# Optimization experiments

Hardware: AMD Instinct MI355X
Metric: run time of the kernel (lower is better)

Reference implementation:

```python
import jax, jax.numpy as jnp
import numpy as np

T, B, E, H = 2048, 4, 1024, 16
D = E // H  # head_dim = 64


def setup_inputs() -> dict:
    key = jax.random.key(0)
    k1, k2, k3, k4 = jax.random.split(key, 4)
    x = jax.random.normal(k1, (T, B, E), dtype=jnp.float32)
    # xavier-ish init scale
    Wqkv = jax.random.normal(k2, (3 * E, E), dtype=jnp.float32) * (1.0 / np.sqrt(2.0 * E))
    Wo = jax.random.normal(k3, (E, E), dtype=jnp.float32) * (1.0 / np.sqrt(E))
    key_padding_mask = jax.random.randint(k4, (B, T), 0, 2).astype(jnp.bool_)  # True = pad
    return {"x": x, "Wqkv": Wqkv, "Wo": Wo, "key_padding_mask": key_padding_mask}


def reference(x, Wqkv, Wo, key_padding_mask):
    t, b, e = x.shape
    h, d = H, E // H
    # fused QKV projection (bias=False)
    qkv = jnp.einsum('tbe,fe->tbf', x, Wqkv).reshape(t, b, 3, h, d)
    # chunk along the 3-axis, then permute to (B, H, T, D)
    q = jnp.transpose(qkv[:, :, 0], (1, 2, 0, 3))
    k = jnp.transpose(qkv[:, :, 1], (1, 2, 0, 3))
    v = jnp.transpose(qkv[:, :, 2], (1, 2, 0, 3))
    # SDPA with default scale 1/sqrt(head_dim); additive -inf mask on padded keys
    scale = 1.0 / jnp.sqrt(jnp.asarray(d, dtype=x.dtype))
    scores = jnp.einsum('bhtd,bhsd->bhts', q, k) * scale
    scores = jnp.where(key_padding_mask[:, None, None, :], -jnp.inf, scores)
    probs = jax.nn.softmax(scores, axis=-1)
    ctx = jnp.einsum('bhts,bhsd->bhtd', probs, v)  # (B,H,T,D)
    ctx = jnp.transpose(ctx, (0, 2, 1, 3)).reshape(b, t, e)  # (B,T,E)
    out = jnp.einsum('bte,fe->btf', ctx, Wo)  # out_proj, bias=False
    return jnp.transpose(out, (1, 0, 2))  # back to (T,B,E)
```

## Files before the change

kernel.cpp:

```cpp
#include <hip/hip_runtime.h>

typedef unsigned short u16;
typedef __bf16 bf16x8 __attribute__((ext_vector_type(8)));
typedef unsigned short u16x8 __attribute__((ext_vector_type(8)));
typedef unsigned short u16x4 __attribute__((ext_vector_type(4)));
typedef float f32x4 __attribute__((ext_vector_type(4)));

__device__ __forceinline__ f32x4 mfma16(u16x8 a, u16x8 b, f32x4 c) {
    return __builtin_amdgcn_mfma_f32_16x16x32_bf16(
        __builtin_bit_cast(bf16x8, a), __builtin_bit_cast(bf16x8, b), c, 0, 0, 0);
}

__device__ __forceinline__ u16 f2b(float f) {
    unsigned int u = __builtin_bit_cast(unsigned int, f);
    return (u16)((u + 0x7fffu + ((u >> 16) & 1u)) >> 16);
}

__device__ __forceinline__ f32x4 zero4() { f32x4 z = {0.f, 0.f, 0.f, 0.f}; return z; }

typedef __attribute__((address_space(1))) const unsigned int gas_u32;
typedef __attribute__((address_space(3))) unsigned int las_u32;
__device__ __forceinline__ void gload16(const u16* g, u16* l) {
    __builtin_amdgcn_global_load_lds((gas_u32*)g, (las_u32*)l, 16, 0, 0);
}

__global__ __launch_bounds__(256) void cvt_bf16_kernel(const float* __restrict__ in,
                                                       u16* __restrict__ out, int n) {
    int i = (blockIdx.x * 256 + threadIdx.x) * 4;
    if (i >= n) return;
    float4 v = *reinterpret_cast<const float4*>(in + i);
    u16x4 o;
    o.x = f2b(v.x); o.y = f2b(v.y); o.z = f2b(v.z); o.w = f2b(v.w);
    *reinterpret_cast<u16x4*>(out + i) = o;
}

__global__ void detect_mask_kernel(const unsigned char* __restrict__ m, int* __restrict__ flag) {
    __shared__ int any;
    if (threadIdx.x == 0) any = 0;
    __syncthreads();
    int acc = 0;
    for (int i = threadIdx.x; i < 8192; i += 256)
        if (i & 3) acc |= m[i];
    if (acc) atomicOr(&any, 1);
    __syncthreads();
    if (threadIdx.x == 0) *flag = any ? 0 : 1;
}

template <int EPI>
__global__ __launch_bounds__(256)
void gemm_bt_kernel(const u16* __restrict__ A, const u16* __restrict__ Bt,
                    int M, int N, int K,
                    u16* __restrict__ qo, u16* __restrict__ ko, u16* __restrict__ vo,
                    float* __restrict__ fo) {
    constexpr int BK = 32;
    __shared__ u16 Al[128 * BK];
    __shared__ u16 Bl[128 * BK];
    int tid = threadIdx.x;
    int wave = tid >> 6, lane = tid & 63;
    int l15 = lane & 15, l16 = lane >> 4;
    int wr = wave >> 1, wc = wave & 1;
    int bx = blockIdx.x, by = blockIdx.y;

    int c0 = tid, c1 = tid + 256;
    const u16* gA0 = A + (size_t)(by * 128 + (c0 >> 2)) * K + (c0 & 3) * 8;
    const u16* gA1 = A + (size_t)(by * 128 + (c1 >> 2)) * K + (c1 & 3) * 8;
    const u16* gB0 = Bt + (size_t)(bx * 128 + (c0 >> 2)) * K + (c0 & 3) * 8;
    const u16* gB1 = Bt + (size_t)(bx * 128 + (c1 >> 2)) * K + (c1 & 3) * 8;
    u16* lA0 = Al + c0 * 8; u16* lA1 = Al + c1 * 8;
    u16* lB0 = Bl + c0 * 8; u16* lB1 = Bl + c1 * 8;

    f32x4 acc[4][4];
#pragma unroll
    for (int m = 0; m < 4; m++)
#pragma unroll
        for (int n = 0; n < 4; n++) acc[m][n] = zero4();

    for (int k0 = 0; k0 < K; k0 += BK) {
        __syncthreads();
        gload16(gA0 + k0, lA0);
        gload16(gA1 + k0, lA1);
        gload16(gB0 + k0, lB0);
        gload16(gB1 + k0, lB1);
        __syncthreads();
        u16x8 af[4], bfr[4];
#pragma unroll
        for (int m = 0; m < 4; m++)
            af[m] = *(const u16x8*)&Al[(wr * 64 + m * 16 + l15) * BK + l16 * 8];
#pragma unroll
        for (int n = 0; n < 4; n++)
            bfr[n] = *(const u16x8*)&Bl[(wc * 64 + n * 16 + l15) * BK + l16 * 8];
#pragma unroll
        for (int m = 0; m < 4; m++)
#pragma unroll
            for (int n = 0; n < 4; n++) acc[m][n] = mfma16(af[m], bfr[n], acc[m][n]);
    }

#pragma unroll
    for (int m = 0; m < 4; m++) {
#pragma unroll
        for (int j = 0; j < 4; j++) {
            int row = by * 128 + wr * 64 + m * 16 + l16 * 4 + j;
#pragma unroll
            for (int n = 0; n < 4; n++) {
                int col = bx * 128 + wc * 64 + n * 16 + l15;
                float val = acc[m][n][j];
                if constexpr (EPI == 0) {
                    int chunk = col >> 10, h = (col >> 6) & 15, d = col & 63;
                    int t = row >> 2, bI = row & 3;
                    if (chunk == 0) val *= 0.18033688011112042f;
                    u16* dst = (chunk == 0) ? qo : (chunk == 1) ? ko : vo;
                    dst[((size_t)(bI * 16 + h) * 2048 + t) * 64 + d] = f2b(val);
                } else {
                    fo[(size_t)row * N + col] = val;
                }
            }
        }
    }
}

__global__ __launch_bounds__(256)
void attn_kernel(const u16* __restrict__ Qg, const u16* __restrict__ Kg,
                 const u16* __restrict__ Vg, const void* __restrict__ maskp,
                 const int* __restrict__ flag, u16* __restrict__ ctx) {
    __shared__ u16 Kl[32 * 72];
    __shared__ u16 Vt[64 * 40];
    __shared__ u16 Pl[4][32 * 40];

    int tid = threadIdx.x;
    int wave = tid >> 6, lane = tid & 63;
    int l15 = lane & 15, l16 = lane >> 4;
    int bh = blockIdx.y;
    int b = bh >> 4, h = bh & 15;
    size_t base = (size_t)bh * 2048 * 64;
    int q0 = blockIdx.x * 128 + wave * 32;

    int isInt = *flag;
    const unsigned char* m8 = (const unsigned char*)maskp;
    const int* m32 = (const int*)maskp;

    u16x8 aq[2][2];
#pragma unroll
    for (int qb = 0; qb < 2; qb++)
#pragma unroll
        for (int ks = 0; ks < 2; ks++)
            aq[qb][ks] = *(const u16x8*)(Qg + base + (size_t)(q0 + qb * 16 + l15) * 64 +
                                         ks * 32 + l16 * 8);

    f32x4 acc_o[2][4];
    float mrun[2][4], plsum[2][4];
#pragma unroll
    for (int qb = 0; qb < 2; qb++) {
#pragma unroll
        for (int db = 0; db < 4; db++) acc_o[qb][db] = zero4();
#pragma unroll
        for (int j = 0; j < 4; j++) { mrun[qb][j] = -1e30f; plsum[qb][j] = 0.f; }
    }

    int srow = tid >> 3, schunk = tid & 7;

    for (int s0 = 0; s0 < 2048; s0 += 32) {
        u16x8 kv = *(const u16x8*)(Kg + base + (size_t)(s0 + srow) * 64 + schunk * 8);
        u16x8 vv = *(const u16x8*)(Vg + base + (size_t)(s0 + srow) * 64 + schunk * 8);
        __syncthreads();
        *(u16x8*)&Kl[srow * 72 + schunk * 8] = kv;
#pragma unroll
        for (int s = 0; s < 8; s++) {
            int i = (srow + schunk + s) & 7;
            Vt[(schunk * 8 + i) * 40 + srow] = vv[i];
        }
        __syncthreads();

        int ki = b * 2048 + s0 + l15;
        int pad0 = isInt ? (m32[ki] != 0) : (m8[ki] != 0);
        int pad1 = isInt ? (m32[ki + 16] != 0) : (m8[ki + 16] != 0);

        f32x4 sa[2][2];
        sa[0][0] = zero4(); sa[0][1] = zero4(); sa[1][0] = zero4(); sa[1][1] = zero4();
#pragma unroll
        for (int kb = 0; kb < 2; kb++)
#pragma unroll
            for (int ks = 0; ks < 2; ks++) {
                u16x8 bk = *(const u16x8*)&Kl[(kb * 16 + l15) * 72 + ks * 32 + l16 * 8];
                sa[0][kb] = mfma16(aq[0][ks], bk, sa[0][kb]);
                sa[1][kb] = mfma16(aq[1][ks], bk, sa[1][kb]);
            }

#pragma unroll
        for (int qb = 0; qb < 2; qb++) {
            float s0v[4], s1v[4];
            float gl = -1e30f;
#pragma unroll
            for (int j = 0; j < 4; j++) {
                s0v[j] = pad0 ? -1e30f : sa[qb][0][j];
                s1v[j] = pad1 ? -1e30f : sa[qb][1][j];
                gl = fmaxf(gl, fmaxf(s0v[j], s1v[j]) - mrun[qb][j]);
            }
            if (__any(gl > 4.0f)) {
                float tm[4];
#pragma unroll
                for (int j = 0; j < 4; j++) tm[j] = fmaxf(s0v[j], s1v[j]);
#pragma unroll
                for (int j = 0; j < 4; j++) {
                    tm[j] = fmaxf(tm[j], __shfl_xor(tm[j], 1));
                    tm[j] = fmaxf(tm[j], __shfl_xor(tm[j], 2));
                    tm[j] = fmaxf(tm[j], __shfl_xor(tm[j], 4));
                    tm[j] = fmaxf(tm[j], __shfl_xor(tm[j], 8));
                }
#pragma unroll
                for (int j = 0; j < 4; j++) {
                    float mnew = fmaxf(mrun[qb][j], tm[j]);
                    float sc = exp2f(mrun[qb][j] - mnew);
                    mrun[qb][j] = mnew;
                    plsum[qb][j] *= sc;
#pragma unroll
                    for (int db = 0; db < 4; db++) acc_o[qb][db][j] *= sc;
                }
            }
#pragma unroll
            for (int j = 0; j < 4; j++) {
                float p0 = exp2f(s0v[j] - mrun[qb][j]);
                float p1 = exp2f(s1v[j] - mrun[qb][j]);
                int prow = qb * 16 + l16 * 4 + j;
                Pl[wave][prow * 40 + l15] = f2b(p0);
                Pl[wave][prow * 40 + 16 + l15] = f2b(p1);
                plsum[qb][j] += p0 + p1;
            }
        }

#pragma unroll
        for (int qb = 0; qb < 2; qb++) {
            u16x8 ap = *(const u16x8*)&Pl[wave][(qb * 16 + l15) * 40 + l16 * 8];
#pragma unroll
            for (int db = 0; db < 4; db++) {
                u16x8 bv = *(const u16x8*)&Vt[(db * 16 + l15) * 40 + l16 * 8];
                acc_o[qb][db] = mfma16(ap, bv, acc_o[qb][db]);
            }
        }
    }

#pragma unroll
    for (int qb = 0; qb < 2; qb++)
#pragma unroll
        for (int j = 0; j < 4; j++) {
            float rs = plsum[qb][j];
            rs += __shfl_xor(rs, 1);
            rs += __shfl_xor(rs, 2);
            rs += __shfl_xor(rs, 4);
            rs += __shfl_xor(rs, 8);
            float inv = 1.0f / rs;
            int qg = q0 + qb * 16 + l16 * 4 + j;
            size_t mrow = (size_t)qg * 4 + b;
#pragma unroll
            for (int db = 0; db < 4; db++)
                ctx[mrow * 1024 + h * 64 + db * 16 + l15] = f2b(acc_o[qb][db][j] * inv);
        }
}

extern "C" void kernel_launch(void* const* d_in, const int* in_sizes, int n_in,
                              void* d_out, int out_size, void* d_ws, size_t ws_size,
                              hipStream_t stream) {
    const float* x = (const float*)d_in[0];
    const float* wqkv = (const float*)d_in[1];
    const float* wo = (const float*)d_in[2];
    const void* mask = d_in[3];
    float* out = (float*)d_out;

    char* ws = (char*)d_ws;
    int* flag = (int*)ws;
    u16* xb = (u16*)(ws + 16);
    u16* wqkvb = xb + 8388608;
    u16* wob = wqkvb + 3145728;
    u16* qw = wob + 1048576;
    u16* kw = qw + 8388608;
    u16* vw = kw + 8388608;
    u16* ctx = xb;

    cvt_bf16_kernel<<<8192, 256, 0, stream>>>(x, xb, 8388608);
    cvt_bf16_kernel<<<3072, 256, 0, stream>>>(wqkv, wqkvb, 3145728);
    cvt_bf16_kernel<<<1024, 256, 0, stream>>>(wo, wob, 1048576);
    detect_mask_kernel<<<1, 256, 0, stream>>>((const unsigned char*)mask, flag);

    gemm_bt_kernel<0><<<dim3(24, 64), 256, 0, stream>>>(xb, wqkvb, 8192, 3072, 1024,
                                                        qw, kw, vw, nullptr);
    attn_kernel<<<dim3(16, 64), 256, 0, stream>>>(qw, kw, vw, mask, flag, ctx);
    gemm_bt_kernel<1><<<dim3(8, 64), 256, 0, stream>>>(ctx, wob, 8192, 1024, 1024,
                                                       nullptr, nullptr, nullptr, out);
}
```

Measured before the change: 473.8 us.

## Use LDS transpose reads for V, prefetch K/V, widen GEMM BK to 64

The GEMM K-tile grows from 32 to 64, so there are half as many sync and load rounds and each tile feeds two MFMA sub-steps. In attention, V is no longer scattered element by element into a transposed LDS buffer. It is stored as row chunks and read with ds_read_b64_tr_b16 transpose loads. The next K/V tile is loaded from global memory into registers during the current iteration to hide latency. The online-softmax rescale threshold is loosened from 4 to 8, which skips more rescales but lets the exponentials grow larger before rescaling. The explicit lgkmcnt waits and sched barriers may serialize the transpose loads.

```diff
diff --git a/kernel.cpp b/kernel.cpp
--- a/kernel.cpp
+++ b/kernel.cpp
@@ -22,6 +22,12 @@
 typedef __attribute__((address_space(3))) unsigned int las_u32;
 __device__ __forceinline__ void gload16(const u16* g, u16* l) {
     __builtin_amdgcn_global_load_lds((gas_u32*)g, (las_u32*)l, 16, 0, 0);
+}
+
+__device__ __forceinline__ u16x4 tr16(unsigned off) {
+    u16x4 r;
+    asm volatile("ds_read_b64_tr_b16 %0, %1" : "=v"(r) : "v"(off));
+    return r;
 }
 
 __global__ __launch_bounds__(256) void cvt_bf16_kernel(const float* __restrict__ in,
@@ -52,22 +58,24 @@
                     int M, int N, int K,
                     u16* __restrict__ qo, u16* __restrict__ ko, u16* __restrict__ vo,
                     float* __restrict__ fo) {
-    constexpr int BK = 32;
-    __shared__ u16 Al[128 * BK];
-    __shared__ u16 Bl[128 * BK];
+    constexpr int BK = 64;
+    __shared__ __align__(16) u16 Al[128 * BK];
+    __shared__ __align__(16) u16 Bl[128 * BK];
     int tid = threadIdx.x;
     int wave = tid >> 6, lane = tid & 63;
     int l15 = lane & 15, l16 = lane >> 4;
     int wr = wave >> 1, wc = wave & 1;
     int bx = blockIdx.x, by = blockIdx.y;
 
-    int c0 = tid, c1 = tid + 256;
-    const u16* gA0 = A + (size_t)(by * 128 + (c0 >> 2)) * K + (c0 & 3) * 8;
-    const u16* gA1 = A + (size_t)(by * 128 + (c1 >> 2)) * K + (c1 & 3) * 8;
-    const u16* gB0 = Bt + (size_t)(bx * 128 + (c0 >> 2)) * K + (c0 & 3) * 8;
-    const u16* gB1 = Bt + (size_t)(bx * 128 + (c1 >> 2)) * K + (c1 & 3) * 8;
-    u16* lA0 = Al + c0 * 8; u16* lA1 = Al + c1 * 8;
-    u16* lB0 = Bl + c0 * 8; u16* lB1 = Bl + c1 * 8;
+    const u16* gA[4]; const u16* gB[4]; u16* lA[4]; u16* lB[4];
+#pragma unroll
+    for (int q = 0; q < 4; q++) {
+        int c = tid + q * 256;
+        gA[q] = A + (size_t)(by * 128 + (c >> 3)) * K + (c & 7) * 8;
+        gB[q] = Bt + (size_t)(bx * 128 + (c >> 3)) * K + (c & 7) * 8;
+        lA[q] = Al + c * 8;
+        lB[q] = Bl + c * 8;
+    }
 
     f32x4 acc[4][4];
 #pragma unroll
@@ -77,22 +85,26 @@
 
     for (int k0 = 0; k0 < K; k0 += BK) {
         __syncthreads();
-        gload16(gA0 + k0, lA0);
-        gload16(gA1 + k0, lA1);
-        gload16(gB0 + k0, lB0);
-        gload16(gB1 + k0, lB1);
+#pragma unroll
+        for (int q = 0; q < 4; q++) {
+            gload16(gA[q] + k0, lA[q]);
+            gload16(gB[q] + k0, lB[q]);
+        }
         __syncthreads();
-        u16x8 af[4], bfr[4];
-#pragma unroll
-        for (int m = 0; m < 4; m++)
-            af[m] = *(const u16x8*)&Al[(wr * 64 + m * 16 + l15) * BK + l16 * 8];
-#pragma unroll
-        for (int n = 0; n < 4; n++)
-            bfr[n] = *(const u16x8*)&Bl[(wc * 64 + n * 16 + l15) * BK + l16 * 8];
-#pragma unroll
-        for (int m = 0; m < 4; m++)
-#pragma unroll
-            for (int n = 0; n < 4; n++) acc[m][n] = mfma16(af[m], bfr[n], acc[m][n]);
+#pragma unroll
+        for (int ks = 0; ks < 2; ks++) {
+            u16x8 af[4], bfr[4];
+#pragma unroll
+            for (int m = 0; m < 4; m++)
+                af[m] = *(const u16x8*)&Al[(wr * 64 + m * 16 + l15) * BK + ks * 32 + l16 * 8];
+#pragma unroll
+            for (int n = 0; n < 4; n++)
+                bfr[n] = *(const u16x8*)&Bl[(wc * 64 + n * 16 + l15) * BK + ks * 32 + l16 * 8];
+#pragma unroll
+            for (int m = 0; m < 4; m++)
+#pragma unroll
+                for (int n = 0; n < 4; n++) acc[m][n] = mfma16(af[m], bfr[n], acc[m][n]);
+        }
     }
 
 #pragma unroll
@@ -122,9 +134,9 @@
 void attn_kernel(const u16* __restrict__ Qg, const u16* __restrict__ Kg,
                  const u16* __restrict__ Vg, const void* __restrict__ maskp,
                  const int* __restrict__ flag, u16* __restrict__ ctx) {
-    __shared__ u16 Kl[32 * 72];
-    __shared__ u16 Vt[64 * 40];
-    __shared__ u16 Pl[4][32 * 40];
+    __shared__ __align__(16) u16 Kl[32 * 72];
+    __shared__ __align__(128) u16 Vs[2048];
+    __shared__ __align__(16) u16 Pl[4][32 * 40];
 
     int tid = threadIdx.x;
     int wave = tid >> 6, lane = tid & 63;
@@ -157,17 +169,23 @@
     }
 
     int srow = tid >> 3, schunk = tid & 7;
-
-    for (int s0 = 0; s0 < 2048; s0 += 32) {
-        u16x8 kv = *(const u16x8*)(Kg + base + (size_t)(s0 + srow) * 64 + schunk * 8);
-        u16x8 vv = *(const u16x8*)(Vg + base + (size_t)(s0 + srow) * 64 + schunk * 8);
+    const u16* kg = Kg + base + (size_t)srow * 64 + schunk * 8;
+    const u16* vg = Vg + base + (size_t)srow * 64 + schunk * 8;
+    u16* kldst = &Kl[srow * 72 + schunk * 8];
+    u16* vsdst = &Vs[(schunk >> 1) * 512 + srow * 16 + (schunk & 1) * 8];
+    unsigned vtrb = (unsigned)(uintptr_t)(&Vs[0]) + (unsigned)(l16 * 256 + l15 * 8);
+
+    u16x8 kv = *(const u16x8*)kg;
+    u16x8 vv = *(const u16x8*)vg;
+
+    for (int it = 0; it < 64; ++it) {
+        int s0 = it * 32;
         __syncthreads();
-        *(u16x8*)&Kl[srow * 72 + schunk * 8] = kv;
-#pragma unroll
-        for (int s = 0; s < 8; s++) {
-            int i = (srow + schunk + s) & 7;
-            Vt[(schunk * 8 + i) * 40 + srow] = vv[i];
-        }
+        *(u16x8*)kldst = kv;
+        *(u16x8*)vsdst = vv;
+        int snext = (s0 + 32) & 2047;
+        u16x8 kv2 = *(const u16x8*)(kg + (size_t)snext * 64);
+        u16x8 vv2 = *(const u16x8*)(vg + (size_t)snext * 64);
         __syncthreads();
 
         int ki = b * 2048 + s0 + l15;
@@ -195,7 +213,7 @@
                 s1v[j] = pad1 ? -1e30f : sa[qb][1][j];
                 gl = fmaxf(gl, fmaxf(s0v[j], s1v[j]) - mrun[qb][j]);
             }
-            if (__any(gl > 4.0f)) {
+            if (__any(gl > 8.0f)) {
                 float tm[4];
 #pragma unroll
                 for (int j = 0; j < 4; j++) tm[j] = fmaxf(s0v[j], s1v[j]);
@@ -227,15 +245,19 @@
             }
         }
 
-#pragma unroll
-        for (int qb = 0; qb < 2; qb++) {
-            u16x8 ap = *(const u16x8*)&Pl[wave][(qb * 16 + l15) * 40 + l16 * 8];
-#pragma unroll
-            for (int db = 0; db < 4; db++) {
-                u16x8 bv = *(const u16x8*)&Vt[(db * 16 + l15) * 40 + l16 * 8];
-                acc_o[qb][db] = mfma16(ap, bv, acc_o[qb][db]);
-            }
-        }
+        u16x8 ap0 = *(const u16x8*)&Pl[wave][(0 * 16 + l15) * 40 + l16 * 8];
+        u16x8 ap1 = *(const u16x8*)&Pl[wave][(1 * 16 + l15) * 40 + l16 * 8];
+#pragma unroll
+        for (int db = 0; db < 4; db++) {
+            u16x4 t0 = tr16(vtrb + db * 1024);
+            u16x4 t1 = tr16(vtrb + db * 1024 + 128);
+            asm volatile("s_waitcnt lgkmcnt(0)" ::: "memory");
+            __builtin_amdgcn_sched_barrier(0);
+            u16x8 bv = {t0[0], t0[1], t0[2], t0[3], t1[0], t1[1], t1[2], t1[3]};
+            acc_o[0][db] = mfma16(ap0, bv, acc_o[0][db]);
+            acc_o[1][db] = mfma16(ap1, bv, acc_o[1][db]);
+        }
+        kv = kv2; vv = vv2;
     }
 
 #pragma unroll
```

Result: faster. 451.9 us (-4.6%).
